# Kernel tuning notes

Measured on AMD Instinct MI355X. Metric: run time of the kernel, lower is better.

## Reference

```python
import jax, jax.numpy as jnp
import numpy as np

N_EMBD = 1024
N_HEAD = 16
B, T = 4, 2048

def setup_inputs() -> dict:
    key = jax.random.key(0)
    ks = jax.random.split(key, 5)
    C = N_EMBD
    s = 0.02
    return {
        "x": jax.random.normal(ks[0], (B, T, C), dtype=jnp.float32),
        "W_attn": jax.random.normal(ks[1], (C, 3 * C), dtype=jnp.float32) * s,
        "b_attn": jnp.zeros((3 * C,), dtype=jnp.float32),
        "W_proj": jax.random.normal(ks[2], (C, C), dtype=jnp.float32) * s,
        "b_proj": jnp.zeros((C,), dtype=jnp.float32),
    }

def reference(x, W_attn, b_attn, W_proj, b_proj):
    Bz, Tz, C = x.shape
    H = N_HEAD
    hd = C // H
    qkv = x @ W_attn + b_attn                      # [B,T,3C]
    q, k, v = jnp.split(qkv, 3, axis=-1)
    # [B,H,T,hd]
    q = q.reshape(Bz, Tz, H, hd).transpose(0, 2, 1, 3)
    k = k.reshape(Bz, Tz, H, hd).transpose(0, 2, 1, 3)
    v = v.reshape(Bz, Tz, H, hd).transpose(0, 2, 1, 3)
    att = jnp.einsum('bhqd,bhkd->bhqk', q, k) * (1.0 / np.sqrt(hd))
    causal = jnp.tril(jnp.ones((Tz, Tz), dtype=bool))
    att = jnp.where(causal, att, -jnp.inf)
    att = jax.nn.softmax(att, axis=-1)
    y = jnp.einsum('bhqk,bhkd->bhqd', att, v)      # [B,H,T,hd]
    y = y.transpose(0, 2, 1, 3).reshape(Bz, Tz, C)
    return y @ W_proj + b_proj
```

## Files before the change

### kernel.cpp

```cpp
#include <hip/hip_runtime.h>
#include <hip/hip_bf16.h>

#define NEMBD 1024
#define NHEAD 16
#define HD    64
#define BB    4
#define TT    2048
#define MM    (BB*TT)
#define NQKV  (3*NEMBD)

typedef unsigned short u16;
typedef __attribute__((ext_vector_type(8))) short short8;
typedef __attribute__((ext_vector_type(4))) float floatx4;

__device__ __forceinline__ u16 f2bf(float f) {
    __hip_bfloat16 h = __float2bfloat16(f);
    return *reinterpret_cast<u16*>(&h);
}

__device__ __forceinline__ unsigned pack_bf16(float a, float b) {
    __hip_bfloat162 h2 = __float22bfloat162_rn(float2{a, b});
    return *reinterpret_cast<unsigned*>(&h2);
}

__device__ __forceinline__ unsigned trunc_pack(float a, float b) {
    return __builtin_amdgcn_perm(__float_as_uint(b), __float_as_uint(a), 0x07060302u);
}

__device__ __forceinline__ void gl_lds16(const u16* g, u16* l) {
    __builtin_amdgcn_global_load_lds(
        (const __attribute__((address_space(1))) unsigned int*)g,
        (__attribute__((address_space(3))) unsigned int*)l,
        16, 0, 0);
}

__device__ __forceinline__ short8 scale8(short8 f, float c) {
    union { short8 s; unsigned u[4]; } a, r;
    a.s = f;
    for (int i = 0; i < 4; i++) {
        float lo = __uint_as_float(a.u[i] << 16) * c;
        float hi = __uint_as_float(a.u[i] & 0xffff0000u) * c;
        r.u[i] = pack_bf16(lo, hi);
    }
    return r.s;
}

__global__ __launch_bounds__(256) void cast_f32_bf16(const float* __restrict__ in,
                                                     u16* __restrict__ out, int n) {
    int i = (blockIdx.x * 256 + threadIdx.x) * 4;
    if (i < n) {
        float4 v = *(const float4*)(in + i);
        uint2 o;
        o.x = pack_bf16(v.x, v.y);
        o.y = pack_bf16(v.z, v.w);
        *(uint2*)(out + i) = o;
    }
}

__global__ __launch_bounds__(256) void transpose_cast(const float* __restrict__ in,
                                                      u16* __restrict__ out, int K, int N) {
    __shared__ float tile[32][33];
    int n0 = blockIdx.x * 32, k0 = blockIdx.y * 32;
    int tx = threadIdx.x, ty = threadIdx.y;
    for (int i = 0; i < 4; i++)
        tile[ty + i * 8][tx] = in[(k0 + ty + i * 8) * N + n0 + tx];
    __syncthreads();
    for (int i = 0; i < 4; i++)
        out[(n0 + ty + i * 8) * K + k0 + tx] = f2bf(tile[tx][ty + i * 8]);
}

template <int EPI>
__global__ __launch_bounds__(256)
void gemm_bt(const u16* __restrict__ A, const u16* __restrict__ Bt,
             const float* __restrict__ bias, void* __restrict__ out0,
             u16* __restrict__ outK, u16* __restrict__ outV) {
    const int K = NEMBD;
    __shared__ u16 As[128 * 32];
    __shared__ u16 Bs[128 * 32];
    int tid = threadIdx.x;
    int lane = tid & 63, w = tid >> 6;
    int quad = lane >> 4, l16 = lane & 15;
    int wm = w >> 1, wn = w & 1;
    int bM = blockIdx.y * 128, bN = blockIdx.x * 128;

    floatx4 acc[4][4];
    for (int i = 0; i < 4; i++)
        for (int j = 0; j < 4; j++)
            acc[i][j] = (floatx4){0.f, 0.f, 0.f, 0.f};

    int srow = lane >> 2, scol = (lane & 3) * 8;
    const u16* Ag0 = A  + (size_t)(bM + w * 32 + srow) * K + scol;
    const u16* Ag1 = A  + (size_t)(bM + w * 32 + 16 + srow) * K + scol;
    const u16* Bg0 = Bt + (size_t)(bN + w * 32 + srow) * K + scol;
    const u16* Bg1 = Bt + (size_t)(bN + w * 32 + 16 + srow) * K + scol;
    u16* LA0 = &As[(w * 32) * 32];
    u16* LA1 = &As[(w * 32 + 16) * 32];
    u16* LB0 = &Bs[(w * 32) * 32];
    u16* LB1 = &Bs[(w * 32 + 16) * 32];

    for (int k0 = 0; k0 < K; k0 += 32) {
        gl_lds16(Ag0 + k0, LA0);
        gl_lds16(Ag1 + k0, LA1);
        gl_lds16(Bg0 + k0, LB0);
        gl_lds16(Bg1 + k0, LB1);
        __syncthreads();
        short8 af[4], bf[4];
        for (int i = 0; i < 4; i++)
            af[i] = *(const short8*)&As[(wm * 64 + i * 16 + l16) * 32 + quad * 8];
        for (int j = 0; j < 4; j++)
            bf[j] = *(const short8*)&Bs[(wn * 64 + j * 16 + l16) * 32 + quad * 8];
        for (int i = 0; i < 4; i++)
            for (int j = 0; j < 4; j++)
                acc[i][j] = __builtin_amdgcn_mfma_f32_16x16x32_bf16(af[i], bf[j], acc[i][j], 0, 0, 0);
        __syncthreads();
    }

    for (int i = 0; i < 4; i++) {
        int mbase = bM + wm * 64 + i * 16 + quad * 4;
        for (int j = 0; j < 4; j++) {
            int n = bN + wn * 64 + j * 16 + l16;
            float bv = bias[n];
            for (int r = 0; r < 4; r++) {
                float v = acc[i][j][r] + bv;
                int mg = mbase + r;
                if (EPI == 0) {
                    int which = n >> 10, c = n & 1023;
                    int h = c >> 6, d = c & 63;
                    int b = mg >> 11, t = mg & 2047;
                    u16* dst = (which == 0) ? (u16*)out0 : (which == 1 ? outK : outV);
                    dst[(((size_t)(b * NHEAD + h) * TT) + t) * HD + d] = f2bf(v);
                } else {
                    ((float*)out0)[(size_t)mg * NEMBD + n] = v;
                }
            }
        }
    }
}

__global__ __launch_bounds__(256, 2)
void attn_kernel(const u16* __restrict__ Q, const u16* __restrict__ Kg,
                 const u16* __restrict__ V, u16* __restrict__ Y) {
    __shared__ u16 Ks[64][72];
    __shared__ u16 Vt[64][72];
    __shared__ u16 Ps[4][32][72];

    int tid = threadIdx.x;
    int lane = tid & 63, w = tid >> 6;
    int quad = lane >> 4, l16 = lane & 15;
    int bh = blockIdx.y;
    int ib = blockIdx.x;
    int qa0 = ib * 128;
    int qb0 = (15 - ib) * 128;
    const u16* Qb = Q  + (size_t)bh * TT * HD;
    const u16* Kb = Kg + (size_t)bh * TT * HD;
    const u16* Vb = V  + (size_t)bh * TT * HD;
    int wqa = qa0 + w * 32;
    int wqb = qb0 + w * 32;

    const float C = 0.18033688f;

    short8 qfa[2][2], qfb[2][2];
    for (int qt = 0; qt < 2; qt++)
        for (int kd = 0; kd < 2; kd++) {
            qfa[qt][kd] = scale8(*(const short8*)(Qb + (size_t)(wqa + qt * 16 + l16) * HD + kd * 32 + quad * 8), C);
            qfb[qt][kd] = scale8(*(const short8*)(Qb + (size_t)(wqb + qt * 16 + l16) * HD + kd * 32 + quad * 8), C);
        }

    floatx4 oa[4][2], ob[4][2];
    for (int dt = 0; dt < 4; dt++)
        for (int qt = 0; qt < 2; qt++) {
            oa[dt][qt] = (floatx4){0.f, 0.f, 0.f, 0.f};
            ob[dt][qt] = (floatx4){0.f, 0.f, 0.f, 0.f};
        }
    float la[2] = {0.f, 0.f};
    float lb[2] = {0.f, 0.f};

    int krow = tid >> 2, kcg = (tid & 3) * 16;
    int vkp = (tid & 31) * 2, vd0 = (tid >> 5) * 8;

    auto process = [&](int k0, int wq0, short8 (&qf)[2][2], short8 (&kf)[4][2],
                       floatx4 (&o)[4][2], float (&l_s)[2]) {
        floatx4 s[2][4];
        for (int qt = 0; qt < 2; qt++)
            for (int kt = 0; kt < 4; kt++) {
                floatx4 a = (floatx4){0.f, 0.f, 0.f, 0.f};
                a = __builtin_amdgcn_mfma_f32_16x16x32_bf16(kf[kt][0], qf[qt][0], a, 0, 0, 0);
                a = __builtin_amdgcn_mfma_f32_16x16x32_bf16(kf[kt][1], qf[qt][1], a, 0, 0, 0);
                s[qt][kt] = a;
            }

        bool diag = (k0 + 64 > wq0);
        for (int qt = 0; qt < 2; qt++) {
            int qg = wq0 + qt * 16 + l16;
            if (diag) {
                for (int kt = 0; kt < 4; kt++)
                    for (int r = 0; r < 4; r++)
                        if (k0 + kt * 16 + quad * 4 + r > qg) s[qt][kt][r] = -INFINITY;
            }
            float rs = 0.f;
            for (int kt = 0; kt < 4; kt++)
                for (int r = 0; r < 4; r++) {
                    float p = exp2f(s[qt][kt][r]);
                    s[qt][kt][r] = p;
                    rs += p;
                }
            l_s[qt] += rs;
        }

        for (int qt = 0; qt < 2; qt++)
            for (int kt = 0; kt < 4; kt++) {
                floatx4 p = s[qt][kt];
                *(unsigned*)&Ps[w][qt * 16 + l16][kt * 16 + quad * 4]     = trunc_pack(p[0], p[1]);
                *(unsigned*)&Ps[w][qt * 16 + l16][kt * 16 + quad * 4 + 2] = trunc_pack(p[2], p[3]);
            }
        short8 pfrag[2][2];
        for (int qt = 0; qt < 2; qt++)
            for (int c = 0; c < 2; c++)
                pfrag[qt][c] = *(const short8*)&Ps[w][qt * 16 + l16][c * 32 + quad * 8];
        for (int c = 0; c < 2; c++)
            for (int dt = 0; dt < 4; dt++) {
                short8 vfrag = *(const short8*)&Vt[dt * 16 + l16][c * 32 + quad * 8];
                for (int qt = 0; qt < 2; qt++)
                    o[dt][qt] = __builtin_amdgcn_mfma_f32_16x16x32_bf16(vfrag, pfrag[qt][c], o[dt][qt], 0, 0, 0);
            }
    };

    int kend = qb0 + 128;
    for (int k0 = 0; k0 < kend; k0 += 64) {
        *(uint4*)&Ks[krow][kcg]     = *(const uint4*)(Kb + (size_t)(k0 + krow) * HD + kcg);
        *(uint4*)&Ks[krow][kcg + 8] = *(const uint4*)(Kb + (size_t)(k0 + krow) * HD + kcg + 8);
        uint4 v0 = *(const uint4*)(Vb + (size_t)(k0 + vkp) * HD + vd0);
        uint4 v1 = *(const uint4*)(Vb + (size_t)(k0 + vkp + 1) * HD + vd0);
        const unsigned* w0p = (const unsigned*)&v0;
        const unsigned* w1p = (const unsigned*)&v1;
        for (int e = 0; e < 4; e++) {
            *(unsigned*)&Vt[vd0 + 2 * e][vkp]     = __builtin_amdgcn_perm(w1p[e], w0p[e], 0x05040100u);
            *(unsigned*)&Vt[vd0 + 2 * e + 1][vkp] = __builtin_amdgcn_perm(w1p[e], w0p[e], 0x07060302u);
        }
        __syncthreads();

        bool acta = (k0 < qa0 + 128) && (k0 < wqa + 32);
        bool actb = (k0 < wqb + 32);
        if (acta || actb) {
            short8 kf[4][2];
            for (int kt = 0; kt < 4; kt++)
                for (int kd = 0; kd < 2; kd++)
                    kf[kt][kd] = *(const short8*)&Ks[kt * 16 + l16][kd * 32 + quad * 8];
            if (acta) process(k0, wqa, qfa, kf, oa, la);
            if (actb) process(k0, wqb, qfb, kf, ob, lb);
        }
        __syncthreads();
    }

    int b = bh >> 4, h = bh & 15;
    for (int half = 0; half < 2; half++) {
        floatx4 (&o)[4][2] = half ? ob : oa;
        float* l_s = half ? lb : la;
        int wq0 = half ? wqb : wqa;
        for (int qt = 0; qt < 2; qt++) {
            float lt = l_s[qt];
            lt += __shfl_xor(lt, 16, 64);
            lt += __shfl_xor(lt, 32, 64);
            float inv = 1.0f / lt;
            int qg = wq0 + qt * 16 + l16;
            size_t base = ((size_t)(b * TT + qg)) * NEMBD + h * HD;
            for (int dt = 0; dt < 4; dt++) {
                *(unsigned*)&Y[base + dt * 16 + quad * 4]     = pack_bf16(o[dt][qt][0] * inv, o[dt][qt][1] * inv);
                *(unsigned*)&Y[base + dt * 16 + quad * 4 + 2] = pack_bf16(o[dt][qt][2] * inv, o[dt][qt][3] * inv);
            }
        }
    }
}

extern "C" void kernel_launch(void* const* d_in, const int* in_sizes, int n_in,
                              void* d_out, int out_size, void* d_ws, size_t ws_size,
                              hipStream_t stream) {
    const float* x      = (const float*)d_in[0];
    const float* W_attn = (const float*)d_in[1];
    const float* b_attn = (const float*)d_in[2];
    const float* W_proj = (const float*)d_in[3];
    const float* b_proj = (const float*)d_in[4];
    float* out = (float*)d_out;

    char* ws = (char*)d_ws;
    u16* xb  = (u16*)(ws + 0);
    u16* wat = (u16*)(ws + 16777216);
    u16* wpt = (u16*)(ws + 23068672);
    u16* Qb  = (u16*)(ws + 25165824);
    u16* Kb  = (u16*)(ws + 41943040);
    u16* Vb  = (u16*)(ws + 58720256);

    cast_f32_bf16<<<(MM * NEMBD / 4 + 255) / 256, 256, 0, stream>>>(x, xb, MM * NEMBD);
    dim3 tb(32, 8);
    transpose_cast<<<dim3(NQKV / 32, NEMBD / 32), tb, 0, stream>>>(W_attn, wat, NEMBD, NQKV);
    transpose_cast<<<dim3(NEMBD / 32, NEMBD / 32), tb, 0, stream>>>(W_proj, wpt, NEMBD, NEMBD);

    gemm_bt<0><<<dim3(NQKV / 128, MM / 128), 256, 0, stream>>>(xb, wat, b_attn, (void*)Qb, Kb, Vb);
    attn_kernel<<<dim3(8, BB * NHEAD), 256, 0, stream>>>(Qb, Kb, Vb, xb);
    gemm_bt<1><<<dim3(NEMBD / 128, MM / 128), 256, 0, stream>>>(xb, wpt, b_proj, (void*)out, nullptr, nullptr);
}
```

Baseline: 269.4 us.

## Double-buffer K/V tiles in attention and widen GEMM K-step with swizzled LDS

Result: faster. 252.4 us (-6.3%).

```diff
diff --git a/kernel.cpp b/kernel.cpp
--- a/kernel.cpp
+++ b/kernel.cpp
@@ -75,8 +75,8 @@
              const float* __restrict__ bias, void* __restrict__ out0,
              u16* __restrict__ outK, u16* __restrict__ outV) {
     const int K = NEMBD;
-    __shared__ u16 As[128 * 32];
-    __shared__ u16 Bs[128 * 32];
+    __shared__ u16 As[128 * 64];
+    __shared__ u16 Bs[128 * 64];
     int tid = threadIdx.x;
     int lane = tid & 63, w = tid >> 6;
     int quad = lane >> 4, l16 = lane & 15;
@@ -88,30 +88,30 @@
         for (int j = 0; j < 4; j++)
             acc[i][j] = (floatx4){0.f, 0.f, 0.f, 0.f};
 
-    int srow = lane >> 2, scol = (lane & 3) * 8;
-    const u16* Ag0 = A  + (size_t)(bM + w * 32 + srow) * K + scol;
-    const u16* Ag1 = A  + (size_t)(bM + w * 32 + 16 + srow) * K + scol;
-    const u16* Bg0 = Bt + (size_t)(bN + w * 32 + srow) * K + scol;
-    const u16* Bg1 = Bt + (size_t)(bN + w * 32 + 16 + srow) * K + scol;
-    u16* LA0 = &As[(w * 32) * 32];
-    u16* LA1 = &As[(w * 32 + 16) * 32];
-    u16* LB0 = &Bs[(w * 32) * 32];
-    u16* LB1 = &Bs[(w * 32 + 16) * 32];
-
-    for (int k0 = 0; k0 < K; k0 += 32) {
-        gl_lds16(Ag0 + k0, LA0);
-        gl_lds16(Ag1 + k0, LA1);
-        gl_lds16(Bg0 + k0, LB0);
-        gl_lds16(Bg1 + k0, LB1);
+    int srow = lane >> 3;
+    int scol = ((lane & 7) ^ srow) * 8;
+    const u16* Ag = A  + (size_t)(bM + w * 32 + srow) * K + scol;
+    const u16* Bg = Bt + (size_t)(bN + w * 32 + srow) * K + scol;
+    int offk[2];
+    offk[0] = ((quad)     ^ (l16 & 7)) * 8;
+    offk[1] = ((4 + quad) ^ (l16 & 7)) * 8;
+
+    for (int k0 = 0; k0 < K; k0 += 64) {
+        for (int i = 0; i < 4; i++) {
+            gl_lds16(Ag + (size_t)i * 8 * K + k0, &As[(w * 32 + i * 8) * 64]);
+            gl_lds16(Bg + (size_t)i * 8 * K + k0, &Bs[(w * 32 + i * 8) * 64]);
+        }
         __syncthreads();
-        short8 af[4], bf[4];
-        for (int i = 0; i < 4; i++)
-            af[i] = *(const short8*)&As[(wm * 64 + i * 16 + l16) * 32 + quad * 8];
-        for (int j = 0; j < 4; j++)
-            bf[j] = *(const short8*)&Bs[(wn * 64 + j * 16 + l16) * 32 + quad * 8];
-        for (int i = 0; i < 4; i++)
+        for (int kk = 0; kk < 2; kk++) {
+            short8 af[4], bf[4];
+            for (int i = 0; i < 4; i++)
+                af[i] = *(const short8*)&As[(wm * 64 + i * 16 + l16) * 64 + offk[kk]];
             for (int j = 0; j < 4; j++)
-                acc[i][j] = __builtin_amdgcn_mfma_f32_16x16x32_bf16(af[i], bf[j], acc[i][j], 0, 0, 0);
+                bf[j] = *(const short8*)&Bs[(wn * 64 + j * 16 + l16) * 64 + offk[kk]];
+            for (int i = 0; i < 4; i++)
+                for (int j = 0; j < 4; j++)
+                    acc[i][j] = __builtin_amdgcn_mfma_f32_16x16x32_bf16(af[i], bf[j], acc[i][j], 0, 0, 0);
+        }
         __syncthreads();
     }
 
@@ -140,8 +140,8 @@
 __global__ __launch_bounds__(256, 2)
 void attn_kernel(const u16* __restrict__ Q, const u16* __restrict__ Kg,
                  const u16* __restrict__ V, u16* __restrict__ Y) {
-    __shared__ u16 Ks[64][72];
-    __shared__ u16 Vt[64][72];
+    __shared__ u16 Ks[2][64][72];
+    __shared__ u16 Vt[2][64][72];
     __shared__ u16 Ps[4][32][72];
 
     int tid = threadIdx.x;
@@ -178,8 +178,19 @@
     int krow = tid >> 2, kcg = (tid & 3) * 16;
     int vkp = (tid & 31) * 2, vd0 = (tid >> 5) * 8;
 
+    auto stage_write = [&](int bp, uint4 k0v, uint4 k1v, uint4 v0, uint4 v1) {
+        *(uint4*)&Ks[bp][krow][kcg]     = k0v;
+        *(uint4*)&Ks[bp][krow][kcg + 8] = k1v;
+        const unsigned* w0p = (const unsigned*)&v0;
+        const unsigned* w1p = (const unsigned*)&v1;
+        for (int e = 0; e < 4; e++) {
+            *(unsigned*)&Vt[bp][vd0 + 2 * e][vkp]     = __builtin_amdgcn_perm(w1p[e], w0p[e], 0x05040100u);
+            *(unsigned*)&Vt[bp][vd0 + 2 * e + 1][vkp] = __builtin_amdgcn_perm(w1p[e], w0p[e], 0x07060302u);
+        }
+    };
+
     auto process = [&](int k0, int wq0, short8 (&qf)[2][2], short8 (&kf)[4][2],
-                       floatx4 (&o)[4][2], float (&l_s)[2]) {
+                       const u16 (*Vtp)[72], floatx4 (&o)[4][2], float (&l_s)[2]) {
         floatx4 s[2][4];
         for (int qt = 0; qt < 2; qt++)
             for (int kt = 0; kt < 4; kt++) {
@@ -219,25 +230,32 @@
                 pfrag[qt][c] = *(const short8*)&Ps[w][qt * 16 + l16][c * 32 + quad * 8];
         for (int c = 0; c < 2; c++)
             for (int dt = 0; dt < 4; dt++) {
-                short8 vfrag = *(const short8*)&Vt[dt * 16 + l16][c * 32 + quad * 8];
+                short8 vfrag = *(const short8*)&Vtp[dt * 16 + l16][c * 32 + quad * 8];
                 for (int qt = 0; qt < 2; qt++)
                     o[dt][qt] = __builtin_amdgcn_mfma_f32_16x16x32_bf16(vfrag, pfrag[qt][c], o[dt][qt], 0, 0, 0);
             }
     };
 
+    {
+        uint4 k0v = *(const uint4*)(Kb + (size_t)krow * HD + kcg);
+        uint4 k1v = *(const uint4*)(Kb + (size_t)krow * HD + kcg + 8);
+        uint4 v0  = *(const uint4*)(Vb + (size_t)vkp * HD + vd0);
+        uint4 v1  = *(const uint4*)(Vb + (size_t)(vkp + 1) * HD + vd0);
+        stage_write(0, k0v, k1v, v0, v1);
+    }
+    __syncthreads();
+
     int kend = qb0 + 128;
-    for (int k0 = 0; k0 < kend; k0 += 64) {
-        *(uint4*)&Ks[krow][kcg]     = *(const uint4*)(Kb + (size_t)(k0 + krow) * HD + kcg);
-        *(uint4*)&Ks[krow][kcg + 8] = *(const uint4*)(Kb + (size_t)(k0 + krow) * HD + kcg + 8);
-        uint4 v0 = *(const uint4*)(Vb + (size_t)(k0 + vkp) * HD + vd0);
-        uint4 v1 = *(const uint4*)(Vb + (size_t)(k0 + vkp + 1) * HD + vd0);
-        const unsigned* w0p = (const unsigned*)&v0;
-        const unsigned* w1p = (const unsigned*)&v1;
-        for (int e = 0; e < 4; e++) {
-            *(unsigned*)&Vt[vd0 + 2 * e][vkp]     = __builtin_amdgcn_perm(w1p[e], w0p[e], 0x05040100u);
-            *(unsigned*)&Vt[vd0 + 2 * e + 1][vkp] = __builtin_amdgcn_perm(w1p[e], w0p[e], 0x07060302u);
-        }
-        __syncthreads();
+    int p = 0;
+    for (int k0 = 0; k0 < kend; k0 += 64, p ^= 1) {
+        bool pref = (k0 + 64 < kend);
+        uint4 nk0, nk1, nv0, nv1;
+        if (pref) {
+            nk0 = *(const uint4*)(Kb + (size_t)(k0 + 64 + krow) * HD + kcg);
+            nk1 = *(const uint4*)(Kb + (size_t)(k0 + 64 + krow) * HD + kcg + 8);
+            nv0 = *(const uint4*)(Vb + (size_t)(k0 + 64 + vkp) * HD + vd0);
+            nv1 = *(const uint4*)(Vb + (size_t)(k0 + 64 + vkp + 1) * HD + vd0);
+        }
 
         bool acta = (k0 < qa0 + 128) && (k0 < wqa + 32);
         bool actb = (k0 < wqb + 32);
@@ -245,10 +263,12 @@
             short8 kf[4][2];
             for (int kt = 0; kt < 4; kt++)
                 for (int kd = 0; kd < 2; kd++)
-                    kf[kt][kd] = *(const short8*)&Ks[kt * 16 + l16][kd * 32 + quad * 8];
-            if (acta) process(k0, wqa, qfa, kf, oa, la);
-            if (actb) process(k0, wqb, qfb, kf, ob, lb);
-        }
+                    kf[kt][kd] = *(const short8*)&Ks[p][kt * 16 + l16][kd * 32 + quad * 8];
+            if (acta) process(k0, wqa, qfa, kf, Vt[p], oa, la);
+            if (actb) process(k0, wqb, qfb, kf, Vt[p], ob, lb);
+        }
+
+        if (pref) stage_write(p ^ 1, nk0, nk1, nv0, nv1);
         __syncthreads();
     }
 
```
